# Performance work log

Hardware: AMD Instinct MI355X
Metric: run time of the kernel (lower is better)

The kernel has to match this reference:

```python
import jax, jax.numpy as jnp
import numpy as np

W = 0.5
EM_ITER = 5
SCALE = 20.0
N, T, D_IN, D_OUT, K, C1 = 16, 750, 2048, 2048, 8, 21  # C1 = class_num + 1


def l2n(f):
    # torch.norm(p=2, dim=-1, keepdim=True); divide with 1e-9 eps
    return f / (jnp.linalg.norm(f, axis=-1, keepdims=True) + 1e-9)


def setup_inputs() -> dict:
    key = jax.random.key(0)
    ks = jax.random.split(key, 5)
    x = jax.random.normal(ks[0], (N, T, D_IN), dtype=jnp.float32)
    W_emb = jax.random.normal(ks[1], (D_IN, D_OUT), dtype=jnp.float32) * (1.0 / np.sqrt(D_IN))
    b_emb = jnp.zeros((D_OUT,), dtype=jnp.float32)
    mu_param = jax.random.normal(ks[2], (K, D_OUT), dtype=jnp.float32) * 0.02
    ac_center = jax.random.normal(ks[3], (C1, D_OUT), dtype=jnp.float32) * 0.02
    fg_center = -1.0 * ac_center[-1][None, :]
    return {"x": x, "W_emb": W_emb, "b_emb": b_emb, "mu_param": mu_param,
            "ac_center": ac_center, "fg_center": fg_center}


def em(mu, x):
    norm_x = l2n(x)
    for _ in range(EM_ITER):
        norm_mu = l2n(mu)
        z = jax.nn.softmax(jnp.einsum('nkd,ntd->nkt', norm_mu, norm_x) * 5.0, axis=1)
        nz = z / (jnp.sum(z, axis=-1, keepdims=True) + 1e-9)
        mu = jnp.einsum('nkt,ntd->nkd', nz, x)
    return mu


def random_walk(x, y, w):
    n, t, _ = x.shape
    x_n, y_n = l2n(x), l2n(y)
    z = jax.nn.softmax(jnp.einsum('nkd,ntd->nkt', y_n, x_n) * 5.0, axis=1)  # (n,k,t)
    nz = z / (jnp.sum(z, axis=-1, keepdims=True) + 1e-9)
    affinity = jnp.einsum('nkt,nks->nts', z, nz)                             # (n,t,t)
    eye_t = jnp.eye(t, dtype=x.dtype)
    y2x_sum_x = w * jnp.einsum('nkt,nkd->ntd', z, y) + x
    # (I - w^2 A)^{-1} @ y2x_sum_x, expressed as a batched solve (same math as torch.solve)
    refined = (1.0 - w) * jnp.linalg.solve(eye_t[None] - (w * w) * affinity, y2x_sum_x)
    return refined


def prediction_module(x, ac_center, fg_center):
    nx = l2n(x)
    nac = l2n(ac_center)
    nfg = l2n(fg_center)
    frm_scrs = jnp.einsum('ntd,cd->ntc', nx, nac) * SCALE        # (n,t,C1)
    frm_fb = jnp.einsum('ntd,kd->ntk', nx, nfg)[..., 0] * SCALE  # (n,t)
    ca_att = jax.nn.sigmoid(frm_fb)
    cw_att = jax.nn.sigmoid(frm_scrs)
    ca_natt = ca_att / (jnp.sum(ca_att, axis=1, keepdims=True) + 1e-5)
    cw_natt = cw_att / (jnp.sum(cw_att, axis=1, keepdims=True) + 1e-5)
    ca_feat = jnp.einsum('ntd,nt->nd', x, ca_natt)
    cw_feat = jnp.einsum('ntd,ntc->ncd', x, cw_natt)
    ca_scr = jnp.einsum('nd,cd->nc', l2n(ca_feat), nac) * SCALE
    cw_scr = jnp.einsum('ncd,cd->nc', l2n(cw_feat), nac) * SCALE
    return (jax.nn.softmax(ca_scr, axis=-1), jax.nn.softmax(cw_scr, axis=-1), ca_att, frm_scrs)


def forward(x, W_emb, b_emb, mu_param, ac_center, fg_center):
    n = x.shape[0]
    x = jax.nn.relu(x @ W_emb + b_emb)  # feature_embedding (Dropout is identity in eval)
    mu = jnp.broadcast_to(mu_param[None], (n,) + mu_param.shape)
    mu = em(mu, x)
    reallocated_x = random_walk(x, mu, W)
    o_ca, o_cw, o_att, o_frm = prediction_module(x, ac_center, fg_center)
    m_ca, m_cw, m_att, m_frm = prediction_module(reallocated_x, ac_center, fg_center)
    mu_scr = jnp.einsum('nkd,cd->nkc', l2n(mu), l2n(ac_center)) * SCALE
    mu_pred = jax.nn.softmax(mu_scr, axis=-1)
    return (o_ca, o_cw, o_att, o_frm, m_ca, m_cw, m_att, m_frm, x, mu, mu_pred)


def reference(x, W_emb, b_emb, mu_param, ac_center, fg_center):
    return forward(x, W_emb, b_emb, mu_param, ac_center, fg_center)
```

## Files before the change

kernel.cpp:

```cpp
#include <hip/hip_runtime.h>

#define NB 16
#define TT 750
#define DD 2048
#define KK 8
#define CC 21
#define NT 12000

#define MU_CH 16
#define MU_TCH 47

typedef __bf16 bf16;
typedef __attribute__((ext_vector_type(4))) float floatx4;
typedef __attribute__((ext_vector_type(8))) __bf16 bf16x8;
typedef __attribute__((ext_vector_type(4))) __bf16 bf16x4;

__device__ __forceinline__ float wave_allreduce_sum(float v) {
#pragma unroll
  for (int m = 32; m > 0; m >>= 1) v += __shfl_xor(v, m, 64);
  return v;
}

__device__ __forceinline__ void async_lds16(const bf16* g, bf16* l) {
  __builtin_amdgcn_global_load_lds(
      (const __attribute__((address_space(1))) void*)(g),
      (__attribute__((address_space(3))) void*)(l), 16, 0, 0);
}

__global__ __launch_bounds__(256) void k_prep(
    const float* __restrict__ W, bf16* __restrict__ Wt,
    const float* __restrict__ ac, const float* __restrict__ fg,
    float* __restrict__ nacf, bf16* __restrict__ nacb,
    const float* __restrict__ mup, float* __restrict__ nmu, bf16* __restrict__ nmub,
    const float* __restrict__ x, bf16* __restrict__ Ab) {
  int b = blockIdx.x, tid = threadIdx.x;
  __shared__ float tile[32][33];
  __shared__ float sb[4];
  if (b < 4096) {
    int j0 = (b & 63) * 32, k0 = (b >> 6) * 32;
    int tx = tid & 31, ty = tid >> 5;
#pragma unroll
    for (int i = 0; i < 4; i++)
      tile[ty + 8 * i][tx] = W[(size_t)(k0 + ty + 8 * i) * DD + j0 + tx];
    __syncthreads();
#pragma unroll
    for (int i = 0; i < 4; i++)
      Wt[(size_t)(j0 + ty + 8 * i) * DD + k0 + tx] = (bf16)tile[tx][ty + 8 * i];
    return;
  }
  if (b < 4128) {
    int r = b - 4096;
    int d0 = tid * 8;
    if (r >= 22) {
#pragma unroll
      for (int j = 0; j < 8; j++) nacb[(size_t)r * DD + d0 + j] = (bf16)0.f;
      return;
    }
    const float* src = (r < 21) ? (ac + (size_t)r * DD) : fg;
    float v[8];
    floatx4 a = *(const floatx4*)(src + d0);
    floatx4 c = *(const floatx4*)(src + d0 + 4);
    v[0]=a.x; v[1]=a.y; v[2]=a.z; v[3]=a.w; v[4]=c.x; v[5]=c.y; v[6]=c.z; v[7]=c.w;
    float ss = 0.f;
#pragma unroll
    for (int j = 0; j < 8; j++) ss += v[j] * v[j];
    ss = wave_allreduce_sum(ss);
    int lane = tid & 63, wid = tid >> 6;
    if (lane == 0) sb[wid] = ss;
    __syncthreads();
    float inv = 1.f / (sqrtf(sb[0] + sb[1] + sb[2] + sb[3]) + 1e-9f);
#pragma unroll
    for (int j = 0; j < 8; j++) {
      float nv = v[j] * inv;
      nacf[(size_t)r * DD + d0 + j] = nv;
      nacb[(size_t)r * DD + d0 + j] = (bf16)nv;
    }
    return;
  }
  if (b < 4256) {
    int bb = b - 4128;
    int n = bb >> 3, k = bb & 7;
    int lane = tid & 63, wid = tid >> 6;
    const float* p = mup + (size_t)k * DD + tid * 8;
    float v[8];
    floatx4 a = *(const floatx4*)p;
    floatx4 c = *(const floatx4*)(p + 4);
    v[0]=a.x; v[1]=a.y; v[2]=a.z; v[3]=a.w; v[4]=c.x; v[5]=c.y; v[6]=c.z; v[7]=c.w;
    float ss = 0.f;
#pragma unroll
    for (int j = 0; j < 8; j++) ss += v[j] * v[j];
    ss = wave_allreduce_sum(ss);
    if (lane == 0) sb[wid] = ss;
    __syncthreads();
    float inv = 1.f / (sqrtf(sb[0] + sb[1] + sb[2] + sb[3]) + 1e-9f);
    float* q = nmu + (size_t)bb * DD + tid * 8;
    bf16* qb = nmub + (size_t)(n * 16 + k) * DD + tid * 8;
#pragma unroll
    for (int j = 0; j < 8; j++) {
      float nv = v[j] * inv;
      q[j] = nv;
      qb[j] = (bf16)nv;
    }
    return;
  }
  int unit0 = (b - 4256) * 4;
#pragma unroll
  for (int u = 0; u < 4; u++) {
    size_t base = ((size_t)(unit0 + u) * 256 + tid) * 8;
    int row = (int)(base >> 11);
    bf16x8 o = {};
    if (row < NT) {
      floatx4 a = *(const floatx4*)(x + base);
      floatx4 c = *(const floatx4*)(x + base + 4);
      o[0]=(bf16)a.x; o[1]=(bf16)a.y; o[2]=(bf16)a.z; o[3]=(bf16)a.w;
      o[4]=(bf16)c.x; o[5]=(bf16)c.y; o[6]=(bf16)c.z; o[7]=(bf16)c.w;
    }
    *(bf16x8*)(Ab + base) = o;
  }
}

__global__ __launch_bounds__(256) void k_gemm(
    const bf16* __restrict__ Ab, const bf16* __restrict__ Bt,
    const float* __restrict__ bias,
    float* __restrict__ Cout, bf16* __restrict__ Cb, float* __restrict__ rowsq) {
  __shared__ bf16 As[128 * 64];
  __shared__ bf16 Bs[128 * 64];
  int tid = threadIdx.x;
  int bid = blockIdx.x;
  int xcd = bid & 7;
  int j = bid >> 3;
  int n0 = (xcd * 2 + (j >= 94 ? 1 : 0)) * 128;
  int m0 = (j % 94) * 128;
  int wid = tid >> 6, lane = tid & 63;
  int wm = (wid >> 1) * 64, wn = (wid & 1) * 64;
  int lrow = lane & 15, lko = (lane >> 4) * 8;
  int lr7 = lrow & 7;
  floatx4 acc[4][4] = {};
  int crow = tid >> 3;
  int jg = ((tid & 7) ^ (crow & 7)) * 8;
  const bf16* gA = Ab + (size_t)(m0 + crow) * DD + jg;
  const bf16* gB = Bt + (size_t)(n0 + crow) * DD + jg;
  bf16* lA = As + tid * 8;
  bf16* lB = Bs + tid * 8;
  for (int k0 = 0; k0 < DD; k0 += 64) {
#pragma unroll
    for (int s = 0; s < 4; s++)
      async_lds16(gA + (size_t)(32 * s) * DD + k0, lA + 2048 * s);
#pragma unroll
    for (int s = 0; s < 4; s++)
      async_lds16(gB + (size_t)(32 * s) * DD + k0, lB + 2048 * s);
    __syncthreads();
#pragma unroll
    for (int ks = 0; ks < 64; ks += 32) {
      bf16x8 af[4], bfr[4];
#pragma unroll
      for (int i = 0; i < 4; i++) {
        int sw = (((ks + lko) >> 3) ^ lr7) * 8;
        af[i] = *(const bf16x8*)(As + (wm + i * 16 + lrow) * 64 + sw);
      }
#pragma unroll
      for (int jj = 0; jj < 4; jj++) {
        int sw = (((ks + lko) >> 3) ^ lr7) * 8;
        bfr[jj] = *(const bf16x8*)(Bs + (wn + jj * 16 + lrow) * 64 + sw);
      }
#pragma unroll
      for (int i = 0; i < 4; i++)
#pragma unroll
        for (int jj = 0; jj < 4; jj++)
          acc[i][jj] = __builtin_amdgcn_mfma_f32_16x16x32_bf16(af[i], bfr[jj], acc[i][jj], 0, 0, 0);
    }
    __syncthreads();
  }
  int quad = lane >> 4;
  float bv[4];
#pragma unroll
  for (int jj = 0; jj < 4; jj++) bv[jj] = bias[n0 + wn + jj * 16 + lrow];
#pragma unroll
  for (int i = 0; i < 4; i++) {
#pragma unroll
    for (int r = 0; r < 4; r++) {
      int row = m0 + wm + i * 16 + quad * 4 + r;
      bool ok = (row < NT);
      float sq = 0.f;
#pragma unroll
      for (int jj = 0; jj < 4; jj++) {
        int col = n0 + wn + jj * 16 + lrow;
        float v = acc[i][jj][r] + bv[jj];
        v = fmaxf(v, 0.f);
        if (ok) {
          Cout[(size_t)row * DD + col] = v;
          Cb[(size_t)row * DD + col] = (bf16)v;
        }
        sq += v * v;
      }
#pragma unroll
      for (int m = 1; m < 16; m <<= 1) sq += __shfl_xor(sq, m, 64);
      if (ok && lrow == 0) atomicAdd(&rowsq[row], sq);
    }
  }
}

__global__ __launch_bounds__(256) void k_score(
    const bf16* __restrict__ Xb, const bf16* __restrict__ nmub,
    const float* __restrict__ rowsq,
    float* __restrict__ z, float* __restrict__ rowsum) {
  __shared__ bf16 As[2][64 * 256];
  __shared__ bf16 Bs[2][16 * 256];
  int tid = threadIdx.x, lane = tid & 63, w = tid >> 6;
  int m0 = blockIdx.x * 64, n = blockIdx.y;
  int lrow = lane & 15, lko = (lane >> 4) * 8, lr7 = lrow & 7;
  int scg = tid & 31;
  int srow = tid >> 5;
  const bf16* gXn = Xb + (size_t)(n * TT + m0) * DD;
  const bf16* gBn = nmub + (size_t)(n * 16) * DD;
#pragma unroll
  for (int r = 0; r < 8; r++) {
    int row = r * 8 + srow;
    int cgg = (scg & 24) | ((scg & 7) ^ (row & 7));
    async_lds16(gXn + (size_t)row * DD + cgg * 8, &As[0][r * 2048 + tid * 8]);
  }
#pragma unroll
  for (int r = 0; r < 2; r++) {
    int row = r * 8 + srow;
    int cgg = (scg & 24) | ((scg & 7) ^ (row & 7));
    async_lds16(gBn + (size_t)row * DD + cgg * 8, &Bs[0][r * 2048 + tid * 8]);
  }
  floatx4 acc = {};
  int buf = 0;
  for (int k0 = 0; k0 < DD; k0 += 256) {
    __syncthreads();
    if (k0 + 256 < DD) {
#pragma unroll
      for (int r = 0; r < 8; r++) {
        int row = r * 8 + srow;
        int cgg = (scg & 24) | ((scg & 7) ^ (row & 7));
        async_lds16(gXn + (size_t)row * DD + k0 + 256 + cgg * 8,
                    &As[buf ^ 1][r * 2048 + tid * 8]);
      }
#pragma unroll
      for (int r = 0; r < 2; r++) {
        int row = r * 8 + srow;
        int cgg = (scg & 24) | ((scg & 7) ^ (row & 7));
        async_lds16(gBn + (size_t)row * DD + k0 + 256 + cgg * 8,
                    &Bs[buf ^ 1][r * 2048 + tid * 8]);
      }
    }
    int arow = w * 16 + lrow;
#pragma unroll
    for (int ks = 0; ks < 256; ks += 32) {
      int cg = (ks + lko) >> 3;
      int cgl = (cg & 24) | ((cg & 7) ^ lr7);
      bf16x8 a = *(const bf16x8*)(&As[buf][arow * 256 + cgl * 8]);
      bf16x8 b = *(const bf16x8*)(&Bs[buf][lrow * 256 + cgl * 8]);
      acc = __builtin_amdgcn_mfma_f32_16x16x32_bf16(a, b, acc, 0, 0, 0);
    }
    buf ^= 1;
  }
  int quad = lane >> 4;
  int k = lrow;
  float pacc = 0.f;
#pragma unroll
  for (int r = 0; r < 4; r++) {
    int trow = m0 + w * 16 + quad * 4 + r;
    bool valid = (trow < TT);
    float rq = valid ? rowsq[n * TT + trow] : 1.f;
    float s = acc[r] * (5.f / (sqrtf(rq) + 1e-9f));
    float mx = s;
    mx = fmaxf(mx, __shfl_xor(mx, 1, 64));
    mx = fmaxf(mx, __shfl_xor(mx, 2, 64));
    mx = fmaxf(mx, __shfl_xor(mx, 4, 64));
    float e = __expf(s - mx);
    float se = e;
    se += __shfl_xor(se, 1, 64);
    se += __shfl_xor(se, 2, 64);
    se += __shfl_xor(se, 4, 64);
    float zz = e / se;
    zz = (valid && k < 8) ? zz : 0.f;
    if (valid && k < 8) z[(size_t)(n * TT + trow) * 8 + k] = zz;
    pacc += zz;
  }
  pacc += __shfl_xor(pacc, 16, 64);
  pacc += __shfl_xor(pacc, 32, 64);
  if (lane < 8) atomicAdd(&rowsum[n * 8 + lane], pacc);
}

__global__ __launch_bounds__(256) void k_mu_accum(
    const bf16* __restrict__ Xb, const float* __restrict__ z,
    float* __restrict__ part2) {
  int n = blockIdx.x, tc = blockIdx.y, tid = threadIdx.x;
  int t0 = tc * MU_TCH;
  int tcnt = min(MU_TCH, TT - t0);
  __shared__ float zs[MU_TCH * 8];
  for (int i = tid; i < tcnt * 8; i += 256) zs[i] = z[(size_t)(n * TT + t0) * 8 + i];
  __syncthreads();
  float acc[8][8] = {};
  const bf16* xp = Xb + (size_t)(n * TT + t0) * DD + tid * 8;
  bf16x8 x0 = *(const bf16x8*)xp;
  bf16x8 x1 = (tcnt > 1) ? *(const bf16x8*)(xp + DD) : x0;
  for (int tt = 0; tt < tcnt; tt++) {
    bf16x8 cur = x0;
    x0 = x1;
    if (tt + 2 < tcnt) x1 = *(const bf16x8*)(xp + (size_t)(tt + 2) * DD);
    float xv[8];
#pragma unroll
    for (int j = 0; j < 8; j++) xv[j] = (float)cur[j];
    floatx4 za = *(const floatx4*)&zs[tt * 8];
    floatx4 zb4 = *(const floatx4*)&zs[tt * 8 + 4];
    float zk[8] = {za.x, za.y, za.z, za.w, zb4.x, zb4.y, zb4.z, zb4.w};
#pragma unroll
    for (int k = 0; k < 8; k++)
#pragma unroll
      for (int j = 0; j < 8; j++) acc[k][j] += zk[k] * xv[j];
  }
  float* pb = part2 + ((size_t)(tc * 16 + n) * 8) * DD + tid * 8;
#pragma unroll
  for (int k = 0; k < 8; k++) {
    floatx4 lo = {acc[k][0], acc[k][1], acc[k][2], acc[k][3]};
    floatx4 hi = {acc[k][4], acc[k][5], acc[k][6], acc[k][7]};
    *(floatx4*)(pb + (size_t)k * DD) = lo;
    *(floatx4*)(pb + (size_t)k * DD + 4) = hi;
  }
}

__global__ void k_mu_finish(const float* __restrict__ part2, const float* __restrict__ rs,
                            float* __restrict__ accS_raw, float* __restrict__ mu_ws,
                            float* __restrict__ mu_out, float* __restrict__ nmu_out,
                            bf16* __restrict__ nmub) {
  int b = blockIdx.x;
  int n = b >> 3, k = b & 7;
  int tid = threadIdx.x, lane = tid & 63, wid = tid >> 6;
  int d0 = tid * 8;
  float s[8] = {};
#pragma unroll 4
  for (int c = 0; c < MU_CH; c++) {
    const float* p = part2 + ((size_t)(c * 16 + n) * 8 + k) * DD + d0;
    floatx4 a = *(const floatx4*)p;
    floatx4 cc = *(const floatx4*)(p + 4);
    s[0] += a.x; s[1] += a.y; s[2] += a.z; s[3] += a.w;
    s[4] += cc.x; s[5] += cc.y; s[6] += cc.z; s[7] += cc.w;
  }
  if (accS_raw != nullptr) {
#pragma unroll
    for (int j = 0; j < 8; j++) accS_raw[(size_t)b * DD + d0 + j] = s[j];
    return;
  }
  float invr = 1.f / (rs[b] + 1e-9f);
  float m[8];
#pragma unroll
  for (int j = 0; j < 8; j++) m[j] = s[j] * invr;
#pragma unroll
  for (int j = 0; j < 8; j++) mu_ws[(size_t)b * DD + d0 + j] = m[j];
  if (mu_out != nullptr) {
#pragma unroll
    for (int j = 0; j < 8; j++) mu_out[(size_t)b * DD + d0 + j] = m[j];
  }
  float ss = 0.f;
#pragma unroll
  for (int j = 0; j < 8; j++) ss += m[j] * m[j];
  ss = wave_allreduce_sum(ss);
  __shared__ float sb[4];
  if (lane == 0) sb[wid] = ss;
  __syncthreads();
  float inv = 1.f / (sqrtf(sb[0] + sb[1] + sb[2] + sb[3]) + 1e-9f);
  bf16* qb = nmub + (size_t)(n * 16 + k) * DD + d0;
#pragma unroll
  for (int j = 0; j < 8; j++) {
    float nv = m[j] * inv;
    nmu_out[(size_t)b * DD + d0 + j] = nv;
    qb[j] = (bf16)nv;
  }
}

__global__ void k_wood_mupred(const float* __restrict__ z, const float* __restrict__ rowsum,
                              const float* __restrict__ S, const float* __restrict__ mu,
                              float* __restrict__ G,
                              const float* __restrict__ nmu, const float* __restrict__ nacf,
                              float* __restrict__ mupred) {
  int tid = threadIdx.x;
  if (blockIdx.x >= 16) {
    int b = blockIdx.x - 16;
    int lane = tid & 63, wid = tid >> 6;
    const float* v = nmu + (size_t)b * DD;
    __shared__ float scr[21];
    for (int c = wid; c < 21; c += 4) {
      const float* a = nacf + (size_t)c * DD;
      float s = 0.f;
      for (int i = lane * 4; i < DD; i += 256) {
        floatx4 vv = *(const floatx4*)(v + i);
        floatx4 aa = *(const floatx4*)(a + i);
        s += vv.x * aa.x + vv.y * aa.y + vv.z * aa.z + vv.w * aa.w;
      }
      s = wave_allreduce_sum(s);
      if (lane == 0) scr[c] = s * 20.f;
    }
    __syncthreads();
    if (tid == 0) {
      float mx = scr[0];
      for (int c = 1; c < 21; c++) mx = fmaxf(mx, scr[c]);
      float se = 0.f;
      for (int c = 0; c < 21; c++) se += __expf(scr[c] - mx);
      float inv = 1.f / se;
      for (int c = 0; c < 21; c++) mupred[(size_t)b * 21 + c] = __expf(scr[c] - mx) * inv;
    }
    return;
  }
  int n = blockIdx.x;
  __shared__ float VU[8][8];
  __shared__ float Mi[8][8];
  __shared__ float invrs[8];
  __shared__ float vus[64][4];
  if (tid < 8) invrs[tid] = 1.f / (rowsum[n * 8 + tid] + 1e-9f);
  {
    int pr = tid >> 2, sl = tid & 3;
    int jj = pr >> 3, kk = pr & 7;
    float s = 0.f;
    for (int t = sl; t < TT; t += 4) {
      const float* zp = z + (size_t)(n * TT + t) * 8;
      s += zp[jj] * zp[kk];
    }
    vus[pr][sl] = s;
  }
  __syncthreads();
  if (tid < 64)
    VU[tid >> 3][tid & 7] =
        (vus[tid][0] + vus[tid][1] + vus[tid][2] + vus[tid][3]) * invrs[tid >> 3];
  __syncthreads();
  if (tid == 0) {
    float M[8][16];
    for (int i = 0; i < 8; i++)
      for (int jj = 0; jj < 8; jj++) {
        M[i][jj] = ((i == jj) ? 1.f : 0.f) - 0.25f * VU[i][jj];
        M[i][8 + jj] = (i == jj) ? 1.f : 0.f;
      }
    for (int c = 0; c < 8; c++) {
      float pv = 1.f / M[c][c];
      for (int jj = 0; jj < 16; jj++) M[c][jj] *= pv;
      for (int rr = 0; rr < 8; rr++)
        if (rr != c) {
          float f = M[rr][c];
          for (int jj = 0; jj < 16; jj++) M[rr][jj] -= f * M[c][jj];
        }
    }
    for (int i = 0; i < 8; i++)
      for (int jj = 0; jj < 8; jj++) Mi[i][jj] = M[i][8 + jj];
  }
  __syncthreads();
  const float* mun = mu + (size_t)n * 8 * DD;
  const float* Sn = S + (size_t)n * 8 * DD;
  float* Gn = G + (size_t)n * 8 * DD;
  for (int d = tid; d < DD; d += 256) {
    float m[8], P[8];
#pragma unroll
    for (int k = 0; k < 8; k++) m[k] = mun[k * DD + d];
#pragma unroll
    for (int k = 0; k < 8; k++) {
      float s = 0.f;
#pragma unroll
      for (int jj = 0; jj < 8; jj++) s += VU[k][jj] * m[jj];
      P[k] = 0.5f * s + Sn[k * DD + d] * invrs[k];
    }
#pragma unroll
    for (int jj = 0; jj < 8; jj++) {
      float s = 0.f;
#pragma unroll
      for (int k = 0; k < 8; k++) s += Mi[jj][k] * P[k];
      Gn[jj * DD + d] = 0.5f * (0.5f * m[jj] + 0.25f * s);
    }
  }
}

__global__ __launch_bounds__(256) void k_rw_passC(
    const bf16* __restrict__ Xb, const float* __restrict__ z,
    const float* __restrict__ G, bf16* __restrict__ refb,
    float* __restrict__ invr) {
  int n = blockIdx.x, ch = blockIdx.y, tid = threadIdx.x;
  int lane = tid & 63, wid = tid >> 6;
  int d0 = tid * 8;
  int t0 = ch * 30;
  const float* Gn = G + (size_t)n * 8 * DD;
  float gr[8][8];
#pragma unroll
  for (int k = 0; k < 8; k++) {
    floatx4 a = *(const floatx4*)(Gn + k * DD + d0);
    floatx4 b = *(const floatx4*)(Gn + k * DD + d0 + 4);
    gr[k][0]=a.x; gr[k][1]=a.y; gr[k][2]=a.z; gr[k][3]=a.w;
    gr[k][4]=b.x; gr[k][5]=b.y; gr[k][6]=b.z; gr[k][7]=b.w;
  }
  __shared__ float red[30][4];
  const bf16* xrow = Xb + (size_t)n * TT * DD;
  bf16x8 xg = *(const bf16x8*)(xrow + (size_t)t0 * DD + d0);
  for (int tt = 0; tt < 30; tt++) {
    int t = t0 + tt;
    bf16x8 x8 = xg;
    if (tt + 1 < 30) xg = *(const bf16x8*)(xrow + (size_t)(t + 1) * DD + d0);
    const float* zp = z + (size_t)(n * TT + t) * 8;
    floatx4 za = *(const floatx4*)zp;
    floatx4 zb4 = *(const floatx4*)(zp + 4);
    float zt[8] = {za.x, za.y, za.z, za.w, zb4.x, zb4.y, zb4.z, zb4.w};
    float r[8];
#pragma unroll
    for (int j = 0; j < 8; j++) {
      float s = 0.5f * (float)x8[j];
#pragma unroll
      for (int k = 0; k < 8; k++) s += zt[k] * gr[k][j];
      r[j] = s;
    }
    bf16x8 ro;
#pragma unroll
    for (int j = 0; j < 8; j++) ro[j] = (bf16)r[j];
    *(bf16x8*)(refb + (size_t)(n * TT + t) * DD + d0) = ro;
    float ss = 0.f;
#pragma unroll
    for (int j = 0; j < 8; j++) ss += r[j] * r[j];
    ss = wave_allreduce_sum(ss);
    if (lane == 0) red[tt][wid] = ss;
  }
  __syncthreads();
  if (tid < 30) {
    float tot = red[tid][0] + red[tid][1] + red[tid][2] + red[tid][3];
    invr[n * TT + t0 + tid] = 1.f / (sqrtf(tot) + 1e-9f);
  }
}

__global__ __launch_bounds__(256) void k_pred_p1(
    const bf16* __restrict__ Xb, const bf16* __restrict__ nacb,
    const float* __restrict__ invn, int mode,
    float* __restrict__ out_frm, float* __restrict__ out_att,
    float* __restrict__ natt, float* __restrict__ att_sums) {
  __shared__ bf16 As[2][32 * 256];
  __shared__ bf16 Bs[2][32 * 256];
  __shared__ float ssum[2][32];
  int tid = threadIdx.x, lane = tid & 63, wid = tid >> 6;
  int m0 = blockIdx.x * 32;
  if (tid < 64) ssum[tid >> 5][tid & 31] = 0.f;
  int lrow = lane & 15, lko = (lane >> 4) * 8, lr7 = lrow & 7;
  int r0 = (wid & 1) * 16, c0 = (wid >> 1) * 16;
  int scg = tid & 31;
  int srow = tid >> 5;
  const bf16* gA = Xb + (size_t)m0 * DD;
  const bf16* gB = nacb;
#pragma unroll
  for (int r = 0; r < 4; r++) {
    int row = r * 8 + srow;
    int cgg = (scg & 24) | ((scg & 7) ^ (row & 7));
    async_lds16(gA + (size_t)row * DD + cgg * 8, &As[0][r * 2048 + tid * 8]);
    async_lds16(gB + (size_t)row * DD + cgg * 8, &Bs[0][r * 2048 + tid * 8]);
  }
  floatx4 acc = {};
  int buf = 0;
  for (int k0 = 0; k0 < DD; k0 += 256) {
    __syncthreads();
    if (k0 + 256 < DD) {
#pragma unroll
      for (int r = 0; r < 4; r++) {
        int row = r * 8 + srow;
        int cgg = (scg & 24) | ((scg & 7) ^ (row & 7));
        async_lds16(gA + (size_t)row * DD + k0 + 256 + cgg * 8,
                    &As[buf ^ 1][r * 2048 + tid * 8]);
        async_lds16(gB + (size_t)row * DD + k0 + 256 + cgg * 8,
                    &Bs[buf ^ 1][r * 2048 + tid * 8]);
      }
    }
#pragma unroll
    for (int ks = 0; ks < 256; ks += 32) {
      int cg = (ks + lko) >> 3;
      int cgl = (cg & 24) | ((cg & 7) ^ lr7);
      bf16x8 a = *(const bf16x8*)(&As[buf][(r0 + lrow) * 256 + cgl * 8]);
      bf16x8 b = *(const bf16x8*)(&Bs[buf][(c0 + lrow) * 256 + cgl * 8]);
      acc = __builtin_amdgcn_mfma_f32_16x16x32_bf16(a, b, acc, 0, 0, 0);
    }
    buf ^= 1;
  }
  __syncthreads();
  int quad = lane >> 4;
  int nbase = m0 / TT;
  int c = c0 + lrow;
#pragma unroll
  for (int r = 0; r < 4; r++) {
    int row = m0 + r0 + quad * 4 + r;
    if (c < 22) {
      float iv = mode ? (1.f / (sqrtf(invn[row]) + 1e-9f)) : invn[row];
      float s = acc[r] * iv * 20.f;
      float sg = 1.f / (1.f + __expf(-s));
      int n_loc = row / TT - nbase;
      if (c < 21) out_frm[(size_t)row * 21 + c] = s;
      else out_att[row] = sg;
      natt[(size_t)row * 22 + c] = sg;
      atomicAdd(&ssum[n_loc][c], sg);
    }
  }
  __syncthreads();
  if (tid < 64) {
    int nl = tid >> 5, cs = tid & 31;
    int nn = nbase + nl;
    if (cs < 22 && nn < NB) {
      float v = ssum[nl][cs];
      if (v != 0.f) atomicAdd(&att_sums[nn * 22 + cs], v);
    }
  }
}

__global__ __launch_bounds__(256) void k_pred_p2(
    const bf16* __restrict__ Xb, const float* __restrict__ natt,
    const float* __restrict__ sums, float* __restrict__ partF) {
  int n = blockIdx.x, dh = blockIdx.y, tc = blockIdx.z, tid = threadIdx.x;
  int d = dh * 1024 + tid * 4;
  int t0 = tc * 94;
  int tcnt = min(94, TT - t0);
  __shared__ float sw[94 * 22];
  for (int i = tid; i < tcnt * 22; i += 256) {
    int c = i - (i / 22) * 22;
    sw[i] = natt[(size_t)(n * TT + t0) * 22 + i] / (sums[n * 22 + c] + 1e-5f);
  }
  __syncthreads();
  float ac[22][4] = {};
  const bf16* xrow = Xb + (size_t)n * TT * DD;
  bf16x4 xg = *(const bf16x4*)(xrow + (size_t)t0 * DD + d);
  for (int tt = 0; tt < tcnt; tt++) {
    bf16x4 x4 = xg;
    if (tt + 1 < tcnt) xg = *(const bf16x4*)(xrow + (size_t)(t0 + tt + 1) * DD + d);
    float xv[4] = {(float)x4[0], (float)x4[1], (float)x4[2], (float)x4[3]};
#pragma unroll
    for (int cidx = 0; cidx < 22; cidx++) {
      float w = sw[tt * 22 + cidx];
#pragma unroll
      for (int jj = 0; jj < 4; jj++) ac[cidx][jj] += w * xv[jj];
    }
  }
  float* pb = partF + ((size_t)(n * 8 + tc) * 22) * DD + d;
#pragma unroll
  for (int cidx = 0; cidx < 22; cidx++) {
    floatx4 v = {ac[cidx][0], ac[cidx][1], ac[cidx][2], ac[cidx][3]};
    *(floatx4*)(pb + (size_t)cidx * DD) = v;
  }
}

__global__ void k_pred_final(const float* __restrict__ partF, float* __restrict__ feats,
                             const float* __restrict__ nacf,
                             float* __restrict__ oca, float* __restrict__ ocw) {
  int n = blockIdx.x, tid = threadIdx.x, lane = tid & 63, wid = tid >> 6;
  float* fnw = feats + (size_t)n * 22 * DD;
  const float* pp = partF + ((size_t)n * 8) * (22 * DD);
  for (int i = tid * 4; i < 22 * DD; i += 1024) {
    floatx4 s = {};
#pragma unroll
    for (int tc = 0; tc < 8; tc++) {
      floatx4 v = *(const floatx4*)(pp + (size_t)tc * 22 * DD + i);
      s.x += v.x; s.y += v.y; s.z += v.z; s.w += v.w;
    }
    *(floatx4*)(fnw + i) = s;
  }
  __threadfence_block();
  __syncthreads();
  const float* fn = fnw;
  __shared__ float rnorm[22];
  __shared__ float scr[42];
  for (int r = wid; r < 22; r += 4) {
    const float* fv = fn + (size_t)r * DD;
    float s = 0.f;
    for (int i = lane * 4; i < DD; i += 256) {
      floatx4 v = *(const floatx4*)(fv + i);
      s += v.x * v.x + v.y * v.y + v.z * v.z + v.w * v.w;
    }
    s = wave_allreduce_sum(s);
    if (lane == 0) rnorm[r] = 1.f / (sqrtf(s) + 1e-9f);
  }
  __syncthreads();
  for (int idx = wid; idx < 42; idx += 4) {
    int c = (idx < 21) ? idx : (idx - 21);
    int fr = (idx < 21) ? c : 21;
    const float* fv = fn + (size_t)fr * DD;
    const float* av = nacf + (size_t)c * DD;
    float s = 0.f;
    for (int i = lane * 4; i < DD; i += 256) {
      floatx4 v = *(const floatx4*)(fv + i);
      floatx4 a = *(const floatx4*)(av + i);
      s += v.x * a.x + v.y * a.y + v.z * a.z + v.w * a.w;
    }
    s = wave_allreduce_sum(s);
    if (lane == 0) scr[idx] = s * 20.f * rnorm[fr];
  }
  __syncthreads();
  if (tid < 2) {
    int base = (tid == 0) ? 21 : 0;
    float* dst = ((tid == 0) ? oca : ocw) + (size_t)n * 21;
    float mx = scr[base];
    for (int c = 1; c < 21; c++) mx = fmaxf(mx, scr[base + c]);
    float se = 0.f;
    for (int c = 0; c < 21; c++) se += __expf(scr[base + c] - mx);
    float inv = 1.f / se;
    for (int c = 0; c < 21; c++) dst[c] = __expf(scr[base + c] - mx) * inv;
  }
}

extern "C" void kernel_launch(void* const* d_in, const int* in_sizes, int n_in,
                              void* d_out, int out_size, void* d_ws, size_t ws_size,
                              hipStream_t stream) {
  const float* x_in = (const float*)d_in[0];
  const float* W = (const float*)d_in[1];
  const float* bemb = (const float*)d_in[2];
  const float* mup = (const float*)d_in[3];
  const float* ac = (const float*)d_in[4];
  const float* fg = (const float*)d_in[5];
  float* out = (float*)d_out;

  char* ws = (char*)d_ws;
  bf16* Wt = (bf16*)ws;
  bf16* Xb = (bf16*)(ws + 8388608);
  bf16* Rb = (bf16*)(ws + 57671680);
  bf16* Ab = (bf16*)(ws + 106954752);
  float* part2 = (float*)(ws + 106954752);
  float* partF = (float*)(ws + 106954752);
  bf16* nacb = (bf16*)(ws + 156237824);
  float* f = (float*)(ws + 156368896);
  float* nacf = f;
  float* mu = nacf + 45056;
  float* nmu = mu + 262144;
  bf16* nmub = (bf16*)(nmu + 262144);
  float* accS = nmu + 262144 + 262144;
  float* G = accS + 262144;
  float* z = G + 262144;
  float* natt = z + 96000;
  float* feats = natt + 264000;
  float* invr = feats + 720896;
  float* rowsum = invr + 12032;
  float* asums_o = rowsum + 768;
  float* asums_m = asums_o + 352;
  float* rowsq = asums_m + 352;

  float* o_ca = out;
  float* o_cw = out + 336;
  float* o_att = out + 672;
  float* o_frm = out + 12672;
  float* m_ca = out + 264672;
  float* m_cw = out + 265008;
  float* m_att = out + 265344;
  float* m_frm = out + 277344;
  float* x_out = out + 529344;
  float* mu_out = out + 25105344;
  float* mup_out = out + 25367488;

  hipMemsetAsync(rowsum, 0, (768 + 352 + 352 + 12032) * sizeof(float), stream);
  hipMemsetAsync(nmub, 0, (size_t)NB * 16 * DD * sizeof(bf16), stream);
  k_prep<<<7264, 256, 0, stream>>>(W, Wt, ac, fg, nacf, nacb, mup, nmu, nmub, x_in, Ab);
  k_gemm<<<1504, 256, 0, stream>>>(Ab, Wt, bemb, x_out, Xb, rowsq);
  for (int it = 0; it < 5; it++) {
    bool last = (it == 4);
    k_score<<<dim3(12, 16), 256, 0, stream>>>(Xb, nmub, rowsq, z, rowsum + it * 128);
    k_mu_accum<<<dim3(16, MU_CH), 256, 0, stream>>>(Xb, z, part2);
    k_mu_finish<<<128, 256, 0, stream>>>(part2, rowsum + it * 128, nullptr, mu,
                                         last ? mu_out : nullptr, nmu, nmub);
  }
  k_score<<<dim3(12, 16), 256, 0, stream>>>(Xb, nmub, rowsq, z, rowsum + 5 * 128);
  k_mu_accum<<<dim3(16, MU_CH), 256, 0, stream>>>(Xb, z, part2);
  k_mu_finish<<<128, 256, 0, stream>>>(part2, nullptr, accS, nullptr, nullptr, nullptr, nullptr);
  k_wood_mupred<<<144, 256, 0, stream>>>(z, rowsum + 5 * 128, accS, mu, G, nmu, nacf, mup_out);
  k_rw_passC<<<dim3(16, 25), 256, 0, stream>>>(Xb, z, G, Rb, invr);
  k_pred_p1<<<375, 256, 0, stream>>>(Xb, nacb, rowsq, 1, o_frm, o_att, natt, asums_o);
  k_pred_p2<<<dim3(16, 2, 8), 256, 0, stream>>>(Xb, natt, asums_o, partF);
  k_pred_final<<<16, 256, 0, stream>>>(partF, feats, nacf, o_ca, o_cw);
  k_pred_p1<<<375, 256, 0, stream>>>(Rb, nacb, invr, 0, m_frm, m_att, natt, asums_m);
  k_pred_p2<<<dim3(16, 2, 8), 256, 0, stream>>>(Rb, natt, asums_m, partF);
  k_pred_final<<<16, 256, 0, stream>>>(partF, feats, nacf, m_ca, m_cw);
}
```

Baseline: 889.0 us.

## Restructure embedding GEMM into double-buffered 256x128 tiles with 512-thread blocks

The embedding GEMM moves from 128x128 tiles with 256 threads and one LDS buffer to 256x128 tiles with 512 threads (8 waves) and a double-buffered LDS pipeline. The next K-slice is issued asynchronously while MFMAs run on the current slice, with explicit vmcnt waits, and s_setprio is raised around the MFMA bursts. This targets the load-then-compute serialization of the old loop and increases reuse of B per tile. In exchange it uses more LDS per block (96 KB), has a hand-tuned wait count that must match the number of outstanding loads, and launches only 752 blocks, which may hurt tail balance.

```diff
diff --git a/kernel.cpp b/kernel.cpp
--- a/kernel.cpp
+++ b/kernel.cpp
@@ -119,73 +119,101 @@
   }
 }
 
-__global__ __launch_bounds__(256) void k_gemm(
+__global__ __launch_bounds__(512, 2) void k_gemm(
     const bf16* __restrict__ Ab, const bf16* __restrict__ Bt,
     const float* __restrict__ bias,
     float* __restrict__ Cout, bf16* __restrict__ Cb, float* __restrict__ rowsq) {
-  __shared__ bf16 As[128 * 64];
-  __shared__ bf16 Bs[128 * 64];
+  __shared__ bf16 As[2][256 * 64];
+  __shared__ bf16 Bs[2][128 * 64];
   int tid = threadIdx.x;
   int bid = blockIdx.x;
-  int xcd = bid & 7;
-  int j = bid >> 3;
-  int n0 = (xcd * 2 + (j >= 94 ? 1 : 0)) * 128;
-  int m0 = (j % 94) * 128;
+  int wid2 = (bid & 7) * 94 + (bid >> 3);
+  int mt = wid2 >> 4, nt = wid2 & 15;
+  int m0 = mt * 256, n0 = nt * 128;
   int wid = tid >> 6, lane = tid & 63;
-  int wm = (wid >> 1) * 64, wn = (wid & 1) * 64;
-  int lrow = lane & 15, lko = (lane >> 4) * 8;
-  int lr7 = lrow & 7;
-  floatx4 acc[4][4] = {};
-  int crow = tid >> 3;
-  int jg = ((tid & 7) ^ (crow & 7)) * 8;
-  const bf16* gA = Ab + (size_t)(m0 + crow) * DD + jg;
-  const bf16* gB = Bt + (size_t)(n0 + crow) * DD + jg;
-  bf16* lA = As + tid * 8;
-  bf16* lB = Bs + tid * 8;
-  for (int k0 = 0; k0 < DD; k0 += 64) {
-#pragma unroll
-    for (int s = 0; s < 4; s++)
-      async_lds16(gA + (size_t)(32 * s) * DD + k0, lA + 2048 * s);
-#pragma unroll
-    for (int s = 0; s < 4; s++)
-      async_lds16(gB + (size_t)(32 * s) * DD + k0, lB + 2048 * s);
-    __syncthreads();
-#pragma unroll
-    for (int ks = 0; ks < 64; ks += 32) {
-      bf16x8 af[4], bfr[4];
-#pragma unroll
-      for (int i = 0; i < 4; i++) {
-        int sw = (((ks + lko) >> 3) ^ lr7) * 8;
-        af[i] = *(const bf16x8*)(As + (wm + i * 16 + lrow) * 64 + sw);
+  int wm = (wid >> 2) * 128, wn = (wid & 3) * 32;
+  int lrow = lane & 15, quad = lane >> 4, lr7 = lrow & 7;
+  int srow = tid >> 3;
+  int scg = tid & 7;
+  floatx4 acc[8][2] = {};
+  const bf16* gA = Ab + (size_t)m0 * DD;
+  const bf16* gB = Bt + (size_t)n0 * DD;
+
+  auto STAGE = [&](int b, int k0) {
+#pragma unroll
+    for (int l = 0; l < 4; l++) {
+      int row = l * 64 + srow;
+      int cs = scg ^ (row & 7);
+      async_lds16(gA + (size_t)row * DD + k0 + cs * 8, &As[b][row * 64 + scg * 8]);
+    }
+#pragma unroll
+    for (int l = 0; l < 2; l++) {
+      int row = l * 64 + srow;
+      int cs = scg ^ (row & 7);
+      async_lds16(gB + (size_t)row * DD + k0 + cs * 8, &Bs[b][row * 64 + scg * 8]);
+    }
+  };
+
+  STAGE(0, 0);
+  for (int kt = 0; kt < 32; ++kt) {
+    int p = kt & 1;
+    __builtin_amdgcn_sched_barrier(0);
+    __builtin_amdgcn_s_barrier();
+    if (kt + 1 < 32) {
+      STAGE(p ^ 1, (kt + 1) * 64);
+      asm volatile("s_waitcnt vmcnt(6)" ::: "memory");
+    } else {
+      asm volatile("s_waitcnt vmcnt(0)" ::: "memory");
+    }
+    __builtin_amdgcn_s_barrier();
+    __builtin_amdgcn_sched_barrier(0);
+    bf16x8 bfrag[2][2];
+#pragma unroll
+    for (int ni = 0; ni < 2; ni++)
+#pragma unroll
+      for (int kh = 0; kh < 2; kh++) {
+        int br = wn + ni * 16 + lrow;
+        int cg = kh * 4 + quad;
+        bfrag[ni][kh] = *(const bf16x8*)(&Bs[p][br * 64 + (cg ^ lr7) * 8]);
       }
 #pragma unroll
-      for (int jj = 0; jj < 4; jj++) {
-        int sw = (((ks + lko) >> 3) ^ lr7) * 8;
-        bfr[jj] = *(const bf16x8*)(Bs + (wn + jj * 16 + lrow) * 64 + sw);
-      }
-#pragma unroll
-      for (int i = 0; i < 4; i++)
-#pragma unroll
-        for (int jj = 0; jj < 4; jj++)
-          acc[i][jj] = __builtin_amdgcn_mfma_f32_16x16x32_bf16(af[i], bfr[jj], acc[i][jj], 0, 0, 0);
-    }
-    __syncthreads();
-  }
-  int quad = lane >> 4;
-  float bv[4];
-#pragma unroll
-  for (int jj = 0; jj < 4; jj++) bv[jj] = bias[n0 + wn + jj * 16 + lrow];
-#pragma unroll
-  for (int i = 0; i < 4; i++) {
+    for (int q = 0; q < 4; q++) {
+      bf16x8 afrag[2][2];
+#pragma unroll
+      for (int mi = 0; mi < 2; mi++)
+#pragma unroll
+        for (int kh = 0; kh < 2; kh++) {
+          int ar = wm + q * 32 + mi * 16 + lrow;
+          int cg = kh * 4 + quad;
+          afrag[mi][kh] = *(const bf16x8*)(&As[p][ar * 64 + (cg ^ lr7) * 8]);
+        }
+      __builtin_amdgcn_s_setprio(1);
+#pragma unroll
+      for (int mi = 0; mi < 2; mi++)
+#pragma unroll
+        for (int ni = 0; ni < 2; ni++) {
+          acc[q * 2 + mi][ni] = __builtin_amdgcn_mfma_f32_16x16x32_bf16(
+              afrag[mi][0], bfrag[ni][0], acc[q * 2 + mi][ni], 0, 0, 0);
+          acc[q * 2 + mi][ni] = __builtin_amdgcn_mfma_f32_16x16x32_bf16(
+              afrag[mi][1], bfrag[ni][1], acc[q * 2 + mi][ni], 0, 0, 0);
+        }
+      __builtin_amdgcn_s_setprio(0);
+    }
+  }
+  float bv[2];
+#pragma unroll
+  for (int ni = 0; ni < 2; ni++) bv[ni] = bias[n0 + wn + ni * 16 + lrow];
+#pragma unroll
+  for (int am = 0; am < 8; am++) {
 #pragma unroll
     for (int r = 0; r < 4; r++) {
-      int row = m0 + wm + i * 16 + quad * 4 + r;
+      int row = m0 + wm + (am >> 1) * 32 + (am & 1) * 16 + quad * 4 + r;
       bool ok = (row < NT);
       float sq = 0.f;
 #pragma unroll
-      for (int jj = 0; jj < 4; jj++) {
-        int col = n0 + wn + jj * 16 + lrow;
-        float v = acc[i][jj][r] + bv[jj];
+      for (int ni = 0; ni < 2; ni++) {
+        int col = n0 + wn + ni * 16 + lrow;
+        float v = acc[am][ni][r] + bv[ni];
         v = fmaxf(v, 0.f);
         if (ok) {
           Cout[(size_t)row * DD + col] = v;
@@ -743,7 +771,7 @@
   hipMemsetAsync(rowsum, 0, (768 + 352 + 352 + 12032) * sizeof(float), stream);
   hipMemsetAsync(nmub, 0, (size_t)NB * 16 * DD * sizeof(bf16), stream);
   k_prep<<<7264, 256, 0, stream>>>(W, Wt, ac, fg, nacf, nacb, mup, nmu, nmub, x_in, Ab);
-  k_gemm<<<1504, 256, 0, stream>>>(Ab, Wt, bemb, x_out, Xb, rowsq);
+  k_gemm<<<752, 512, 0, stream>>>(Ab, Wt, bemb, x_out, Xb, rowsq);
   for (int it = 0; it < 5; it++) {
     bool last = (it == 4);
     k_score<<<dim3(12, 16), 256, 0, stream>>>(Xb, nmub, rowsq, z, rowsum + it * 128);
```

Measured after the change: 909.4 us. 1.02x slower.
